# Optimization experiments

Hardware: AMD Instinct MI355X
Metric: run time of the kernel (lower is better)

## Reference

```python
import jax, jax.numpy as jnp
import numpy as np
from jax import lax

H = 100          # hidden_size
IN = 100         # input_size
NUM_LAYERS = 2   # options.LSTMLayer
B = 128
T = 1024


def _uniform(key, shape, bound):
    return jax.random.uniform(key, shape, jnp.float32, -bound, bound)


def setup_inputs() -> dict:
    key = jax.random.key(0)
    ks = jax.random.split(key, 16)
    bound = 1.0 / np.sqrt(H)  # torch nn.LSTM default init
    x = jax.random.normal(ks[0], (B, IN, T), jnp.float32)
    # layer 0: input dim IN; layer 1: input dim 2*H. Stacked over 2 directions.
    w_ih0 = _uniform(ks[1], (2, 4 * H, IN), bound)
    w_hh0 = _uniform(ks[2], (2, 4 * H, H), bound)
    b0 = _uniform(ks[3], (2, 4 * H), bound) + _uniform(ks[4], (2, 4 * H), bound)  # b_ih + b_hh
    w_ih1 = _uniform(ks[5], (2, 4 * H, 2 * H), bound)
    w_hh1 = _uniform(ks[6], (2, 4 * H, H), bound)
    b1 = _uniform(ks[7], (2, 4 * H), bound) + _uniform(ks[8], (2, 4 * H), bound)
    return {"x": x, "w_ih0": w_ih0, "w_hh0": w_hh0, "b0": b0,
            "w_ih1": w_ih1, "w_hh1": w_hh1, "b1": b1}


def _lstm_dir(x, w_ih, w_hh, b):
    # x: (T,B,D). Precompute input-to-gate GEMM once, then scan the recurrence.
    gx = jnp.einsum('tbd,gd->tbg', x, w_ih) + b  # (T,B,4H)
    h0 = jnp.zeros((x.shape[1], H), x.dtype)
    c0 = jnp.zeros((x.shape[1], H), x.dtype)

    def step(carry, g):
        h, c = carry
        gates = g + h @ w_hh.T
        i, f, gg, o = jnp.split(gates, 4, axis=-1)  # torch gate order i,f,g,o
        i = jax.nn.sigmoid(i)
        f = jax.nn.sigmoid(f)
        gg = jnp.tanh(gg)
        o = jax.nn.sigmoid(o)
        c = f * c + i * gg
        h = o * jnp.tanh(c)
        return (h, c), h

    _, hs = lax.scan(step, (h0, c0), gx)
    return hs  # (T,B,H)


def _bilstm_layer(x, w_ih, w_hh, b):
    fwd = _lstm_dir(x, w_ih[0], w_hh[0], b[0])
    bwd = _lstm_dir(x[::-1], w_ih[1], w_hh[1], b[1])[::-1]
    return jnp.concatenate([fwd, bwd], axis=-1)  # (T,B,2H)


def reference(x, w_ih0, w_hh0, b0, w_ih1, w_hh1, b1):
    # x: (B, 100, T) -> permute([2,0,1]) -> (T, B, 100)
    h = jnp.transpose(x, (2, 0, 1))
    h = _bilstm_layer(h, w_ih0, w_hh0, b0)
    h = _bilstm_layer(h, w_ih1, w_hh1, b1)
    return h  # (T, B, 2H), matching nn.LSTM `output`
```

## Files before the change

### kernel.cpp

```cpp
#include <hip/hip_runtime.h>
#include <hip/hip_bf16.h>
#include <stdint.h>

typedef unsigned short ushort_t;
typedef __attribute__((ext_vector_type(8))) short short8;
typedef __attribute__((ext_vector_type(4))) short short4_t;
typedef __attribute__((ext_vector_type(4))) float f32x4;

#define TT 1024
#define BB 128
#define NG 400
#define HID 100

#define ALIGN256(x) ((((size_t)(x)) + 255) & ~(size_t)255)

static const size_t WS_FLAG = 0;
static const size_t WS_XT   = 4096;
static const size_t WS_OUT0 = WS_XT   + (size_t)1024 * 128 * 128 * 2;
static const size_t WS_GX   = WS_OUT0 + (size_t)1024 * 128 * 256 * 2;
static const size_t WS_WIH0 = WS_GX   + (size_t)2 * 1024 * 128 * 400 * 2;
static const size_t WS_WHH  = WS_WIH0 + (size_t)2 * 400 * 128 * 2;
static const size_t WS_WIH1 = WS_WHH  + (size_t)2 * 2 * 400 * 128 * 2;
static const size_t WS_BIAS = WS_WIH1 + (size_t)2 * 400 * 256 * 2;

__device__ __forceinline__ float bf2f(ushort_t v) {
  return __builtin_bit_cast(float, ((unsigned)v) << 16);
}
__device__ __forceinline__ ushort_t f2bf(float f) {
  unsigned u = __builtin_bit_cast(unsigned, f);
  u += 0x7FFF + ((u >> 16) & 1);
  return (ushort_t)(u >> 16);
}
__device__ __forceinline__ ushort_t ldbf(const void* p, size_t i, int isbf) {
  return isbf ? ((const ushort_t*)p)[i] : f2bf(((const float*)p)[i]);
}
__device__ __forceinline__ float ldf(const void* p, size_t i, int isbf) {
  return isbf ? bf2f(((const ushort_t*)p)[i]) : ((const float*)p)[i];
}
__device__ __forceinline__ float fexp2(float x) {
#if __has_builtin(__builtin_amdgcn_exp2f)
  return __builtin_amdgcn_exp2f(x);
#else
  return __exp2f(x);
#endif
}
__device__ __forceinline__ float frcp(float x) {
#if __has_builtin(__builtin_amdgcn_rcpf)
  return __builtin_amdgcn_rcpf(x);
#else
  return 1.0f / x;
#endif
}
__device__ __forceinline__ float sigm(float x) {
  return frcp(1.0f + fexp2(-1.44269504f * x));
}
__device__ __forceinline__ float tanh_(float x) {
  return 1.0f - 2.0f * frcp(1.0f + fexp2(2.88539008f * x));
}

__global__ __launch_bounds__(256) void detect_dtype(const ushort_t* __restrict__ x,
                                                    int* __restrict__ flag) {
  __shared__ int cnt;
  if (threadIdx.x == 0) cnt = 0;
  __syncthreads();
  int local = 0;
  for (int i = threadIdx.x; i < 4096; i += 256) {
    ushort_t u = x[2 * i];
    int e = (u >> 7) & 0xFF;
    if (e >= 0x66 && e <= 0x85) local++;
  }
  atomicAdd(&cnt, local);
  __syncthreads();
  if (threadIdx.x == 0) *flag = (cnt >= 2048) ? 1 : 0;
}

__global__ __launch_bounds__(256) void prep_weights(
    const void* __restrict__ wih0, const void* __restrict__ whh0,
    const void* __restrict__ b0,   const void* __restrict__ wih1,
    const void* __restrict__ whh1, const void* __restrict__ b1,
    ushort_t* __restrict__ WIH0, ushort_t* __restrict__ WHH,
    ushort_t* __restrict__ WIH1, float* __restrict__ BIAS,
    const int* __restrict__ flag)
{
  const int isbf = *flag;
  int tid = blockIdx.x * blockDim.x + threadIdx.x;
  int nth = gridDim.x * blockDim.x;
  for (int idx = tid; idx < 2 * NG * 128; idx += nth) {
    int k = idx & 127; int np = (idx >> 7) % NG; int d = idx / (NG * 128);
    int n = (np & 3) * HID + (np >> 2);
    WIH0[idx] = (k < HID) ? ldbf(wih0, (size_t)(d * NG + n) * 100 + k, isbf) : (ushort_t)0;
  }
  for (int idx = tid; idx < 2 * 2 * NG * 128; idx += nth) {
    int k = idx & 127; int np = (idx >> 7) % NG; int dl = idx / (NG * 128);
    int d = dl & 1; int l = dl >> 1;
    int n = (np & 3) * HID + (np >> 2);
    const void* src = l ? whh1 : whh0;
    WHH[idx] = (k < HID) ? ldbf(src, (size_t)(d * NG + n) * 100 + k, isbf) : (ushort_t)0;
  }
  for (int idx = tid; idx < 2 * NG * 256; idx += nth) {
    int k = idx & 255; int np = (idx >> 8) % NG; int d = idx / (NG * 256);
    int n = (np & 3) * HID + (np >> 2);
    int c = (k < 100) ? k : ((k >= 128 && k < 228) ? (k - 28) : -1);
    WIH1[idx] = (c >= 0) ? ldbf(wih1, (size_t)(d * NG + n) * 200 + c, isbf) : (ushort_t)0;
  }
  for (int idx = tid; idx < 2 * 2 * NG; idx += nth) {
    int np = idx % NG; int dl = idx / NG; int d = dl & 1; int l = dl >> 1;
    int n = (np & 3) * HID + (np >> 2);
    BIAS[idx] = ldf(l ? b1 : b0, d * NG + n, isbf);
  }
}

__global__ __launch_bounds__(256) void pack_x(const void* __restrict__ x,
                                              ushort_t* __restrict__ xT,
                                              const int* __restrict__ flag)
{
  __shared__ ushort_t tile[100][68];
  const int isbf = *flag;
  const int b = blockIdx.x;
  const int t0 = blockIdx.y << 6;
  for (int i = threadIdx.x; i < 100 * 64; i += 256) {
    int k = i >> 6, t = i & 63;
    tile[k][t] = ldbf(x, ((size_t)b * 100 + k) * TT + t0 + t, isbf);
  }
  __syncthreads();
  for (int i = threadIdx.x; i < 128 * 64; i += 256) {
    int k = i & 127, t = i >> 7;
    xT[((size_t)(t0 + t) * BB + b) * 128 + k] = (k < 100) ? tile[k][t] : (ushort_t)0;
  }
}

__global__ __launch_bounds__(256) void gemm_gx(
    const ushort_t* __restrict__ A, const ushort_t* __restrict__ W,
    const float* __restrict__ BIASL, ushort_t* __restrict__ gxo, int kpad)
{
  const int mtile = blockIdx.x;
  const int d = blockIdx.y;
  const int w = threadIdx.x >> 6;
  const int lane = threadIdx.x & 63;
  const int quad = lane >> 4;
  const int lm = lane & 15;
  const int m0 = mtile * 16;
  const int nkt = kpad >> 5;

  f32x4 acc[7];
#pragma unroll
  for (int i = 0; i < 7; i++) acc[i] = (f32x4){0.f, 0.f, 0.f, 0.f};

  const ushort_t* Wd = W + (size_t)d * NG * kpad;
  const ushort_t* Ap = A + (size_t)(m0 + lm) * kpad + quad * 8;

  for (int kt = 0; kt < nkt; kt++) {
    short8 a = *(const short8*)(Ap + kt * 32);
#pragma unroll
    for (int i = 0; i < 7; i++) {
      int nt = w + 4 * i; if (nt >= 25) nt = 0;
      short8 bb = *(const short8*)(Wd + (size_t)(nt * 16 + lm) * kpad + kt * 32 + quad * 8);
      acc[i] = __builtin_amdgcn_mfma_f32_16x16x32_bf16(a, bb, acc[i], 0, 0, 0);
    }
  }

  const int t = mtile >> 3, bg = mtile & 7;
  ushort_t* go = gxo + (((size_t)d * TT + t) * 8 + bg) * 6400;
  const float* bd = BIASL + d * NG;
  const int qr = lm >> 2, gam = lm & 3;
#pragma unroll
  for (int i = 0; i < 7; i++) {
    int nt = w + 4 * i;
    if (nt >= 25) break;
    int n = nt * 16 + lm;
    float bias = bd[n];
#pragma unroll
    for (int r = 0; r < 4; r++)
      go[(nt * 64 + (quad * 4 + r) * 4 + qr) * 4 + gam] = f2bf(acc[i][r] + bias);
  }
}

template<bool F32OUT>
__global__ __launch_bounds__(512, 1) void lstm_layer(
    const ushort_t* __restrict__ gx, const ushort_t* __restrict__ WHHl,
    void* __restrict__ outp, int ostride, int colmult)
{
  const int dir = blockIdx.x >> 3;
  const int bg = blockIdx.x & 7;
  const int b0 = bg << 4;
  const int w = threadIdx.x >> 6;
  const int lane = threadIdx.x & 63;
  const int quad = lane >> 4;
  const int lm = lane & 15;
  const int ocol = dir * colmult;

  __shared__ ushort_t hbuf[2][16][136];
  for (int i = threadIdx.x; i < 2 * 16 * 136; i += 512) ((ushort_t*)hbuf)[i] = 0;

  short8 afragW[4][4];
  int nts[4];
#pragma unroll
  for (int i = 0; i < 4; i++) {
    int nt = (i < 3) ? (w + 8 * i) : 24;
    nts[i] = nt;
    const ushort_t* wp = WHHl + ((size_t)dir * NG + nt * 16 + lm) * 128;
#pragma unroll
    for (int kt = 0; kt < 4; kt++)
      afragW[i][kt] = *(const short8*)(wp + kt * 32 + quad * 8);
  }

  int loff[4];
#pragma unroll
  for (int i = 0; i < 4; i++) loff[i] = (nts[i] * 64 + lm * 4 + quad) * 4;

  float cst[4] = {0.f, 0.f, 0.f, 0.f};
  const ushort_t* gxd = gx + ((size_t)dir * TT * 8 + bg) * 6400;

  short4_t pf[4];
  {
    int tt0 = dir ? (TT - 1) : 0;
    const ushort_t* gp = gxd + (size_t)tt0 * 8 * 6400;
#pragma unroll
    for (int i = 0; i < 4; i++) pf[i] = *(const short4_t*)(gp + loff[i]);
  }

  __syncthreads();

  for (int t = 0; t < TT; t++) {
    const int tt = dir ? (TT - 1 - t) : t;
    const int pb = t & 1;

    f32x4 acc[4];
#pragma unroll
    for (int i = 0; i < 4; i++) {
#pragma unroll
      for (int r = 0; r < 4; r++) acc[i][r] = bf2f((ushort_t)pf[i][r]);
    }

    if (t + 1 < TT) {
      int tn = dir ? (TT - 2 - t) : (t + 1);
      const ushort_t* gp = gxd + (size_t)tn * 8 * 6400;
#pragma unroll
      for (int i = 0; i < 4; i++) pf[i] = *(const short4_t*)(gp + loff[i]);
    }

    short8 bfr[4];
#pragma unroll
    for (int kt = 0; kt < 4; kt++)
      bfr[kt] = *(const short8*)(&hbuf[pb][lm][kt * 32 + quad * 8]);

#pragma unroll
    for (int i = 0; i < 4; i++) {
      if (i == 3 && w != 0) continue;
#pragma unroll
      for (int kt = 0; kt < 4; kt++)
        acc[i] = __builtin_amdgcn_mfma_f32_16x16x32_bf16(afragW[i][kt], bfr[kt], acc[i], 0, 0, 0);
    }

#pragma unroll
    for (int i = 0; i < 4; i++) {
      if (i == 3 && w != 0) continue;
      float gi = acc[i][0], gf = acc[i][1], gg = acc[i][2], go = acc[i][3];
      float cn = sigm(gf) * cst[i] + sigm(gi) * tanh_(gg);
      cst[i] = cn;
      float h = sigm(go) * tanh_(cn);
      int j = nts[i] * 4 + quad;
      hbuf[pb ^ 1][lm][j] = f2bf(h);
      size_t oidx = ((size_t)tt * BB + b0 + lm) * ostride + ocol + j;
      if (F32OUT) ((float*)outp)[oidx] = h;
      else        ((ushort_t*)outp)[oidx] = f2bf(h);
    }
    __syncthreads();
  }
}

extern "C" void kernel_launch(void* const* d_in, const int* in_sizes, int n_in,
                              void* d_out, int out_size, void* d_ws, size_t ws_size,
                              hipStream_t stream) {
  const void* x_raw    = d_in[0];
  const void* wih0_raw = d_in[1];
  const void* whh0_raw = d_in[2];
  const void* b0_raw   = d_in[3];
  const void* wih1_raw = d_in[4];
  const void* whh1_raw = d_in[5];
  const void* b1_raw   = d_in[6];

  char* ws = (char*)d_ws;
  int*      FLAG = (int*)(ws + WS_FLAG);
  ushort_t* xT   = (ushort_t*)(ws + WS_XT);
  ushort_t* out0 = (ushort_t*)(ws + WS_OUT0);
  ushort_t* gx   = (ushort_t*)(ws + WS_GX);
  ushort_t* WIH0 = (ushort_t*)(ws + WS_WIH0);
  ushort_t* WHH  = (ushort_t*)(ws + WS_WHH);
  ushort_t* WIH1 = (ushort_t*)(ws + WS_WIH1);
  float*    BIAS = (float*)(ws + WS_BIAS);

  detect_dtype<<<1, 256, 0, stream>>>((const ushort_t*)x_raw, FLAG);

  prep_weights<<<256, 256, 0, stream>>>(wih0_raw, whh0_raw, b0_raw,
                                        wih1_raw, whh1_raw, b1_raw,
                                        WIH0, WHH, WIH1, BIAS, FLAG);
  pack_x<<<dim3(128, 16), 256, 0, stream>>>(x_raw, xT, FLAG);

  gemm_gx<<<dim3(8192, 2), 256, 0, stream>>>(xT, WIH0, BIAS, gx, 128);
  lstm_layer<false><<<16, 512, 0, stream>>>(gx, WHH, out0, 256, 128);
  gemm_gx<<<dim3(8192, 2), 256, 0, stream>>>(out0, WIH1, BIAS + 2 * NG, gx, 256);
  lstm_layer<true><<<16, 512, 0, stream>>>(gx, WHH + (size_t)2 * NG * 128, d_out, 200, 100);
}
```

Before: 3.039 ms.

## Enlarge gx GEMM tiles, strength-reduce LSTM pointers, swizzle hidden-state LDS

The input GEMM now computes 64 rows per block, reusing each weight fragment across four MFMA row tiles and launching a quarter as many blocks. The recurrent kernel replaces per-step index arithmetic with incrementing pointers for the gate prefetch and output stores. It also XOR-swizzles the shared hidden-state buffer to reduce LDS bank conflicts. The extra accumulators raise register pressure in the GEMM, and prep_weights is launched with twice as many blocks.

```diff
diff --git a/kernel.cpp b/kernel.cpp
--- a/kernel.cpp
+++ b/kernel.cpp
@@ -11,8 +11,6 @@
 #define BB 128
 #define NG 400
 #define HID 100
-
-#define ALIGN256(x) ((((size_t)(x)) + 255) & ~(size_t)255)
 
 static const size_t WS_FLAG = 0;
 static const size_t WS_XT   = 4096;
@@ -133,45 +131,55 @@
     const ushort_t* __restrict__ A, const ushort_t* __restrict__ W,
     const float* __restrict__ BIASL, ushort_t* __restrict__ gxo, int kpad)
 {
-  const int mtile = blockIdx.x;
+  const int blk = blockIdx.x;
   const int d = blockIdx.y;
   const int w = threadIdx.x >> 6;
   const int lane = threadIdx.x & 63;
   const int quad = lane >> 4;
   const int lm = lane & 15;
-  const int m0 = mtile * 16;
+  const int m0 = blk * 64;
   const int nkt = kpad >> 5;
 
-  f32x4 acc[7];
-#pragma unroll
-  for (int i = 0; i < 7; i++) acc[i] = (f32x4){0.f, 0.f, 0.f, 0.f};
+  f32x4 acc[4][7];
+#pragma unroll
+  for (int ms = 0; ms < 4; ms++)
+#pragma unroll
+    for (int i = 0; i < 7; i++) acc[ms][i] = (f32x4){0.f, 0.f, 0.f, 0.f};
 
   const ushort_t* Wd = W + (size_t)d * NG * kpad;
-  const ushort_t* Ap = A + (size_t)(m0 + lm) * kpad + quad * 8;
 
   for (int kt = 0; kt < nkt; kt++) {
-    short8 a = *(const short8*)(Ap + kt * 32);
+    short8 a[4];
+#pragma unroll
+    for (int ms = 0; ms < 4; ms++)
+      a[ms] = *(const short8*)(A + (size_t)(m0 + ms * 16 + lm) * kpad + kt * 32 + quad * 8);
 #pragma unroll
     for (int i = 0; i < 7; i++) {
       int nt = w + 4 * i; if (nt >= 25) nt = 0;
       short8 bb = *(const short8*)(Wd + (size_t)(nt * 16 + lm) * kpad + kt * 32 + quad * 8);
-      acc[i] = __builtin_amdgcn_mfma_f32_16x16x32_bf16(a, bb, acc[i], 0, 0, 0);
-    }
-  }
-
-  const int t = mtile >> 3, bg = mtile & 7;
-  ushort_t* go = gxo + (((size_t)d * TT + t) * 8 + bg) * 6400;
+#pragma unroll
+      for (int ms = 0; ms < 4; ms++)
+        acc[ms][i] = __builtin_amdgcn_mfma_f32_16x16x32_bf16(a[ms], bb, acc[ms][i], 0, 0, 0);
+    }
+  }
+
+  const int t = blk >> 1;
   const float* bd = BIASL + d * NG;
   const int qr = lm >> 2, gam = lm & 3;
 #pragma unroll
-  for (int i = 0; i < 7; i++) {
-    int nt = w + 4 * i;
-    if (nt >= 25) break;
-    int n = nt * 16 + lm;
-    float bias = bd[n];
-#pragma unroll
-    for (int r = 0; r < 4; r++)
-      go[(nt * 64 + (quad * 4 + r) * 4 + qr) * 4 + gam] = f2bf(acc[i][r] + bias);
+  for (int ms = 0; ms < 4; ms++) {
+    const int bg = (blk & 1) * 4 + ms;
+    ushort_t* go = gxo + (((size_t)d * TT + t) * 8 + bg) * 6400;
+#pragma unroll
+    for (int i = 0; i < 7; i++) {
+      int nt = w + 4 * i;
+      if (nt >= 25) break;
+      int n = nt * 16 + lm;
+      float bias = bd[n];
+#pragma unroll
+      for (int r = 0; r < 4; r++)
+        go[(nt * 64 + (quad * 4 + r) * 4 + qr) * 4 + gam] = f2bf(acc[ms][i][r] + bias);
+    }
   }
 }
 
@@ -188,6 +196,7 @@
   const int quad = lane >> 4;
   const int lm = lane & 15;
   const int ocol = dir * colmult;
+  const int esz = F32OUT ? 4 : 2;
 
   __shared__ ushort_t hbuf[2][16][136];
   for (int i = threadIdx.x; i < 2 * 16 * 136; i += 512) ((ushort_t*)hbuf)[i] = 0;
@@ -204,25 +213,31 @@
       afragW[i][kt] = *(const short8*)(wp + kt * 32 + quad * 8);
   }
 
-  int loff[4];
-#pragma unroll
-  for (int i = 0; i < 4; i++) loff[i] = (nts[i] * 64 + lm * 4 + quad) * 4;
-
   float cst[4] = {0.f, 0.f, 0.f, 0.f};
+  const int t0 = dir ? (TT - 1) : 0;
+
   const ushort_t* gxd = gx + ((size_t)dir * TT * 8 + bg) * 6400;
-
+  const long gstep = dir ? -(long)(8 * 6400) : (long)(8 * 6400);
+  const ushort_t* gp[4];
   short4_t pf[4];
-  {
-    int tt0 = dir ? (TT - 1) : 0;
-    const ushort_t* gp = gxd + (size_t)tt0 * 8 * 6400;
-#pragma unroll
-    for (int i = 0; i < 4; i++) pf[i] = *(const short4_t*)(gp + loff[i]);
-  }
+#pragma unroll
+  for (int i = 0; i < 4; i++) {
+    gp[i] = gxd + (size_t)t0 * 8 * 6400 + (nts[i] * 64 + lm * 4 + quad) * 4;
+    pf[i] = *(const short4_t*)gp[i];
+  }
+
+  const long odelta = (long)(dir ? -BB : BB) * ostride * esz;
+  char* op[4];
+#pragma unroll
+  for (int i = 0; i < 4; i++)
+    op[i] = (char*)outp +
+            (((size_t)t0 * BB + b0 + lm) * ostride + ocol + nts[i] * 4 + quad) * esz;
+
+  const int rsw = 8 * (quad ^ (lm & 3));
 
   __syncthreads();
 
   for (int t = 0; t < TT; t++) {
-    const int tt = dir ? (TT - 1 - t) : t;
     const int pb = t & 1;
 
     f32x4 acc[4];
@@ -233,16 +248,14 @@
     }
 
     if (t + 1 < TT) {
-      int tn = dir ? (TT - 2 - t) : (t + 1);
-      const ushort_t* gp = gxd + (size_t)tn * 8 * 6400;
-#pragma unroll
-      for (int i = 0; i < 4; i++) pf[i] = *(const short4_t*)(gp + loff[i]);
+#pragma unroll
+      for (int i = 0; i < 4; i++) { gp[i] += gstep; pf[i] = *(const short4_t*)gp[i]; }
     }
 
     short8 bfr[4];
 #pragma unroll
     for (int kt = 0; kt < 4; kt++)
-      bfr[kt] = *(const short8*)(&hbuf[pb][lm][kt * 32 + quad * 8]);
+      bfr[kt] = *(const short8*)(&hbuf[pb][lm][kt * 32 + rsw]);
 
 #pragma unroll
     for (int i = 0; i < 4; i++) {
@@ -259,11 +272,12 @@
       float cn = sigm(gf) * cst[i] + sigm(gi) * tanh_(gg);
       cst[i] = cn;
       float h = sigm(go) * tanh_(cn);
+      ushort_t hb = f2bf(h);
       int j = nts[i] * 4 + quad;
-      hbuf[pb ^ 1][lm][j] = f2bf(h);
-      size_t oidx = ((size_t)tt * BB + b0 + lm) * ostride + ocol + j;
-      if (F32OUT) ((float*)outp)[oidx] = h;
-      else        ((ushort_t*)outp)[oidx] = f2bf(h);
+      hbuf[pb ^ 1][lm][j ^ (8 * (lm & 3))] = hb;
+      if (F32OUT) *(float*)op[i] = h;
+      else        *(ushort_t*)op[i] = hb;
+      op[i] += odelta;
     }
     __syncthreads();
   }
@@ -292,13 +306,13 @@
 
   detect_dtype<<<1, 256, 0, stream>>>((const ushort_t*)x_raw, FLAG);
 
-  prep_weights<<<256, 256, 0, stream>>>(wih0_raw, whh0_raw, b0_raw,
+  prep_weights<<<512, 256, 0, stream>>>(wih0_raw, whh0_raw, b0_raw,
                                         wih1_raw, whh1_raw, b1_raw,
                                         WIH0, WHH, WIH1, BIAS, FLAG);
   pack_x<<<dim3(128, 16), 256, 0, stream>>>(x_raw, xT, FLAG);
 
-  gemm_gx<<<dim3(8192, 2), 256, 0, stream>>>(xT, WIH0, BIAS, gx, 128);
+  gemm_gx<<<dim3(2048, 2), 256, 0, stream>>>(xT, WIH0, BIAS, gx, 128);
   lstm_layer<false><<<16, 512, 0, stream>>>(gx, WHH, out0, 256, 128);
-  gemm_gx<<<dim3(8192, 2), 256, 0, stream>>>(out0, WIH1, BIAS + 2 * NG, gx, 256);
+  gemm_gx<<<dim3(2048, 2), 256, 0, stream>>>(out0, WIH1, BIAS + 2 * NG, gx, 256);
   lstm_layer<true><<<16, 512, 0, stream>>>(gx, WHH + (size_t)2 * NG * 128, d_out, 200, 100);
 }
```

Result: slower. 3.398 ms (+11.8%).
